# Optimization experiments

Hardware: AMD Instinct MI355X
Metric: run time of the kernel (lower is better)

Reference implementation:

```python
import jax, jax.numpy as jnp
import numpy as np

SIGNAL = (32, 32)
KERNEL = (8, 8)
N_FEATURES = [64, 128, 128]
BATCH = 64
ALPHA = 0.5          # source references an undefined global `alpha`; fixed here
LEAKY_SLOPE = 0.01   # torch F.leaky_relu default


def _join_tensor(S, K, loc):
    i = np.arange(S)[:, None, None]
    j = np.arange(S)[None, :, None]
    k = np.arange(K)[None, None, :]
    M = (j >= i) & (i == np.maximum(j, k + loc))
    return jnp.asarray(M.astype(np.float32))


def _meet_tensor(S, K, loc):
    i = np.arange(S)[:, None, None]
    j = np.arange(S)[None, :, None]
    k = np.arange(K)[None, None, :]
    M = (j >= i) & (i == np.minimum(j, k + loc))
    return jnp.asarray(M.astype(np.float32))


def setup_inputs() -> dict:
    key = jax.random.key(0)
    sx, sy = SIGNAL
    kx, ky = KERNEL
    # meet layers use kernel_loc = signal - kernel; join layers use (0, 0)
    cmx = _meet_tensor(sx, kx, sx - kx)
    cmy = _meet_tensor(sy, ky, sy - ky)
    cjx = _join_tensor(sx, kx, 0)
    cjy = _join_tensor(sy, ky, 0)

    keys = jax.random.split(key, 16)
    x = jax.random.normal(keys[0], (BATCH, N_FEATURES[0], sx, sy), dtype=jnp.float32)

    def kaiming(k, shape):
        fan_in = shape[0] * shape[1] * shape[2]  # kx*ky*in_features
        return jax.random.normal(k, shape, dtype=jnp.float32) * np.float32(np.sqrt(2.0 / fan_in))

    inp = {"x": x, "cmx": cmx, "cmy": cmy, "cjx": cjx, "cjy": cjy}
    for li in range(len(N_FEATURES) - 1):
        fi, fo = N_FEATURES[li], N_FEATURES[li + 1]
        inp[f"mw{li}"] = kaiming(keys[1 + 2 * li], (kx, ky, fi, fo))
        inp[f"mb{li}"] = jnp.zeros((fo, 1, 1), dtype=jnp.float32)
        inp[f"jw{li}"] = kaiming(keys[2 + 2 * li], (kx, ky, fi, fo))
        inp[f"jb{li}"] = jnp.zeros((fo, 1, 1), dtype=jnp.float32)
    return inp


def _lattice_conv(cx, cy, X, W, b):
    # Y[m,g,x,y] = sum_{i,j,a,b} cx[i,x,a] cy[j,y,b] X[m,f,i,j] W[a,b,f,g] + bias
    return jnp.einsum('ixa,jyb,mfij,abfg->mgxy', cx, cy, X, W, optimize='optimal') + b


def reference(x, cmx, cmy, cjx, cjy, mw0, mb0, jw0, jb0, mw1, mb1, jw1, jb1):
    params = [(mw0, mb0, jw0, jb0), (mw1, mb1, jw1, jb1)]
    for mw, mb, jw, jb in params:
        m = _lattice_conv(cmx, cmy, x, mw, mb)
        j = _lattice_conv(cjx, cjy, x, jw, jb)
        x = jax.nn.leaky_relu((1.0 - ALPHA) * m + ALPHA * j, negative_slope=LEAKY_SLOPE)
    return x
```

## Files before the change

### kernel.cpp

```cpp
#include <hip/hip_runtime.h>
#include <stdint.h>


typedef __attribute__((ext_vector_type(8))) short short8;
typedef __attribute__((ext_vector_type(4))) float floatx4;

__device__ __forceinline__ float bf2f(unsigned short u) {
  union { uint32_t u; float f; } c; c.u = ((uint32_t)u) << 16; return c.f;
}
__device__ __forceinline__ unsigned short f2bf(float f) {
  union { float f; uint32_t u; } c; c.f = f;
  uint32_t u = c.u;
  uint32_t r = (u + 0x7FFFu + ((u >> 16) & 1u)) >> 16;
  return (unsigned short)r;
}

__global__ void detect_and_bias(const unsigned short* __restrict__ xa,
                                const void* __restrict__ mb0,
                                const void* __restrict__ jb0,
                                const void* __restrict__ mb1,
                                const void* __restrict__ jb1,
                                float* __restrict__ bias0,
                                float* __restrict__ bias1,
                                int* __restrict__ flag) {
  __shared__ int cnt;
  if (threadIdx.x == 0) cnt = 0;
  __syncthreads();
  unsigned short v = xa[threadIdx.x];
  int e = (v >> 7) & 0xFF;
  int ok = (v == 0) || (e >= 110 && e <= 140);
  atomicAdd(&cnt, ok);
  __syncthreads();
  int fp32 = (cnt >= 240) ? 0 : 1;
  if (threadIdx.x == 0) *flag = fp32;
  int g = threadIdx.x & 127;
  const void* mb = (threadIdx.x < 128) ? mb0 : mb1;
  const void* jb = (threadIdx.x < 128) ? jb0 : jb1;
  float* bo = (threadIdx.x < 128) ? bias0 : bias1;
  float m = fp32 ? ((const float*)mb)[g] : bf2f(((const unsigned short*)mb)[g]);
  float j = fp32 ? ((const float*)jb)[g] : bf2f(((const unsigned short*)jb)[g]);
  bo[g] = 0.5f * (m + j);
}

__global__ __launch_bounds__(256) void transpose_in(
    const unsigned short* __restrict__ s16, const float* __restrict__ s32,
    unsigned short* __restrict__ dst, int R, int C,
    const int* __restrict__ flag) {
  __shared__ unsigned short tile[32][33];
  int fp32 = *flag;
  int tx = threadIdx.x, ty = threadIdx.y;
  int c0 = blockIdx.x * 32, r0 = blockIdx.y * 32;
  if (fp32) {
#pragma unroll
    for (int i = 0; i < 32; i += 8)
      tile[ty + i][tx] = f2bf(s32[(size_t)(r0 + ty + i) * C + (c0 + tx)]);
  } else {
#pragma unroll
    for (int i = 0; i < 32; i += 8)
      tile[ty + i][tx] = s16[(size_t)(r0 + ty + i) * C + (c0 + tx)];
  }
  __syncthreads();
#pragma unroll
  for (int i = 0; i < 32; i += 8)
    dst[(size_t)(c0 + ty + i) * R + (r0 + tx)] = tile[tx][ty + i];
}

__global__ __launch_bounds__(256) void transpose_out(
    const unsigned short* __restrict__ src, unsigned short* __restrict__ d16,
    float* __restrict__ d32, int R, int C, const int* __restrict__ flag) {
  __shared__ unsigned short tile[32][33];
  int fp32 = *flag;
  int tx = threadIdx.x, ty = threadIdx.y;
  int c0 = blockIdx.x * 32, r0 = blockIdx.y * 32;
#pragma unroll
  for (int i = 0; i < 32; i += 8)
    tile[ty + i][tx] = src[(size_t)(r0 + ty + i) * C + (c0 + tx)];
  __syncthreads();
  if (fp32) {
#pragma unroll
    for (int i = 0; i < 32; i += 8)
      d32[(size_t)(c0 + ty + i) * R + (r0 + tx)] = bf2f(tile[tx][ty + i]);
  } else {
#pragma unroll
    for (int i = 0; i < 32; i += 8)
      d16[(size_t)(c0 + ty + i) * R + (r0 + tx)] = tile[tx][ty + i];
  }
}

#define SLOT_W1 0
#define SLOT_SB 225
#define SLOT_AS 289
#define SLOT_M  353
#define N_SLOTS 417
#define N_SLOTS_PAD 448

__global__ __launch_bounds__(256) void pack_weights(
    const void* __restrict__ mw0, const void* __restrict__ jw0,
    const void* __restrict__ mw1, const void* __restrict__ jw1,
    unsigned short* __restrict__ PB0, unsigned short* __restrict__ PB1,
    const int* __restrict__ flag) {
  int layer = blockIdx.z;
  int FG = layer ? 16384 : 8192;
  int c0 = blockIdx.x * 32;
  if (c0 >= FG) return;
  int kt = blockIdx.y;
  const void* src = (kt < 2) ? (layer ? mw1 : mw0) : (layer ? jw1 : jw0);
  unsigned short* PB = layer ? PB1 : PB0;
  int r0 = (kt & 1) * 32;
  int fp32 = *flag;
  __shared__ unsigned short tile[32][33];
  int tx = threadIdx.x, ty = threadIdx.y;
#pragma unroll
  for (int i = 0; i < 32; i += 8) {
    size_t idx = (size_t)(r0 + ty + i) * FG + (c0 + tx);
    tile[ty + i][tx] = fp32 ? f2bf(((const float*)src)[idx])
                            : ((const unsigned short*)src)[idx];
  }
  __syncthreads();
#pragma unroll
  for (int i = 0; i < 32; i += 8)
    PB[(size_t)(c0 + ty + i) * 128 + (kt * 32 + tx)] = tile[tx][ty + i];
}

__global__ __launch_bounds__(256) void build_L(unsigned short* __restrict__ L) {
  int tid = blockIdx.x * 256 + threadIdx.x;
  int slot = tid >> 7, k = tid & 127;
  int isj = k >= 64, ab = k & 63, a = ab >> 3, b = ab & 7;
  float v = 0.f;
  if (slot < 225) {
    int cx = slot / 15, cy = slot % 15;
    int pmx = cx < 7 ? cx : 7, pxx = cx > 7 ? cx - 7 : 0;
    int pmy = cy < 7 ? cy : 7, pyy = cy > 7 ? cy - 7 : 0;
    if (!isj) v = (a >= pxx && b >= pyy) ? 0.5f : 0.f;
    else      v = (a <= pmx && b <= pmy) ? 0.5f : 0.f;
  } else if (slot < 289) {
    int s = slot - SLOT_SB, px = s >> 3, b0 = s & 7;
    if (!isj) v = (a >= px && b == b0) ? 0.5f : 0.f;
  } else if (slot < 353) {
    int s = slot - SLOT_AS, a0 = s >> 3, py = s & 7;
    if (!isj) v = (a == a0 && b >= py) ? 0.5f : 0.f;
  } else if (slot < 417) {
    int s = slot - SLOT_M, a0 = s >> 3, b0 = s & 7;
    if (!isj) v = (a == a0 && b == b0) ? 0.5f : 0.f;
  }
  L[tid] = f2bf(v);
}

template <int F, int NT>
__device__ __forceinline__ void mfma_tile(
    const unsigned short* __restrict__ A, const unsigned short* __restrict__ W,
    floatx4 acc[NT], int wave, int n, int q) {
  const unsigned short* a_ptr = A + ((size_t)(wave * 16 + n)) * F + q * 8;
  const unsigned short* w_ptr = W + (size_t)n * F + q * 8;
#pragma unroll
  for (int kk = 0; kk < F; kk += 32) {
    short8 av = *(const short8*)(a_ptr + kk);
#pragma unroll
    for (int t = 0; t < NT; ++t) {
      short8 bv = *(const short8*)(w_ptr + (size_t)t * 16 * F + kk);
      acc[t] = __builtin_amdgcn_mfma_f32_16x16x32_bf16(av, bv, acc[t], 0, 0, 0);
    }
  }
}

__global__ __launch_bounds__(256) void prep_gemm(
    const unsigned short* __restrict__ L,
    const unsigned short* __restrict__ PB0,
    const unsigned short* __restrict__ PB1,
    unsigned short* __restrict__ Int0, unsigned short* __restrict__ Int1) {
  int layer = blockIdx.z;
  int FG = layer ? 16384 : 8192;
  int n0 = blockIdx.x * 128;
  if (n0 >= FG) return;
  int m0 = blockIdx.y * 64;
  const unsigned short* PB = layer ? PB1 : PB0;
  unsigned short* Int = layer ? Int1 : Int0;
  int wave = threadIdx.x >> 6, lane = threadIdx.x & 63;
  int n = lane & 15, q = lane >> 4;
  floatx4 acc[8];
#pragma unroll
  for (int t = 0; t < 8; ++t) acc[t] = (floatx4){0.f, 0.f, 0.f, 0.f};
  mfma_tile<128, 8>(L + (size_t)m0 * 128, PB + (size_t)n0 * 128, acc, wave, n, q);
#pragma unroll
  for (int t = 0; t < 8; ++t) {
    int gcol = n0 + t * 16 + n;
#pragma unroll
    for (int r = 0; r < 4; ++r) {
      int m = m0 + wave * 16 + q * 4 + r;
      Int[(size_t)m * FG + gcol] = f2bf(acc[t][r]);
    }
  }
}

__global__ __launch_bounds__(256) void prep_stageB(
    const unsigned short* __restrict__ Int0,
    const unsigned short* __restrict__ Int1,
    unsigned short* __restrict__ Wall0, unsigned short* __restrict__ Wall1) {
  int zz = blockIdx.z;
  int layer = (zz >= N_SLOTS) ? 1 : 0;
  int slot = zz - layer * N_SLOTS;
  int F = layer ? 128 : 64;
  int f0 = blockIdx.y * 32;
  if (f0 >= F) return;
  int g0 = blockIdx.x * 32;
  const unsigned short* src =
      (layer ? Int1 : Int0) + (size_t)slot * F * 128;
  unsigned short* dst = (layer ? Wall1 : Wall0) + (size_t)slot * F * 128;
  __shared__ unsigned short tile[32][33];
  int tx = threadIdx.x, ty = threadIdx.y;
#pragma unroll
  for (int i = 0; i < 32; i += 8)
    tile[ty + i][tx] = src[(size_t)(f0 + ty + i) * 128 + (g0 + tx)];
  __syncthreads();
#pragma unroll
  for (int i = 0; i < 32; i += 8)
    dst[(size_t)(g0 + ty + i) * F + (f0 + tx)] = tile[tx][ty + i];
}

template <int F>
__global__ __launch_bounds__(256) void corr_gemm(
    const unsigned short* __restrict__ Xt, const unsigned short* __restrict__ Wall,
    float* __restrict__ V, float* __restrict__ U, float* __restrict__ T) {
  int bid = blockIdx.x, gs = blockIdx.y;
  int wave = threadIdx.x >> 6, lane = threadIdx.x & 63;
  int n = lane & 15, q = lane >> 4;
  int ipos, slot;
  float* out;
  if (bid < 256) {
    int a = bid >> 5, y = bid & 31;
    int py = y > 24 ? y - 24 : 0;
    ipos = (24 + a) * 32 + y;
    slot = SLOT_AS + a * 8 + py;
    out = V + (size_t)(a * 32 + y) * 8192;
  } else if (bid < 512) {
    int i = bid - 256;
    int b = i >> 5, x = i & 31;
    int px = x > 24 ? x - 24 : 0;
    ipos = x * 32 + 24 + b;
    slot = SLOT_SB + px * 8 + b;
    out = U + (size_t)(b * 32 + x) * 8192;
  } else {
    int i = bid - 512;
    int a = i >> 3, b = i & 7;
    ipos = (24 + a) * 32 + 24 + b;
    slot = SLOT_M + a * 8 + b;
    out = T + (size_t)(a * 8 + b) * 8192;
  }
  floatx4 acc[4];
#pragma unroll
  for (int t = 0; t < 4; ++t) acc[t] = (floatx4){0.f, 0.f, 0.f, 0.f};
  mfma_tile<F, 4>(Xt + (size_t)ipos * 64 * F,
                  Wall + ((size_t)slot * 128 + gs * 64) * F, acc, wave, n, q);
#pragma unroll
  for (int t = 0; t < 4; ++t) {
    int gcol = gs * 64 + t * 16 + n;
#pragma unroll
    for (int r = 0; r < 4; ++r) {
      int m = wave * 16 + q * 4 + r;
      out[(size_t)m * 128 + gcol] = acc[t][r];
    }
  }
}

__global__ __launch_bounds__(256) void scan_corr(float* __restrict__ V,
                                                 float* __restrict__ U,
                                                 float* __restrict__ T) {
  int b = blockIdx.x;
  if (b < 2048) {
    float* base = (b < 1024) ? V : U;
    int tid = ((b & 1023) * 256 + threadIdx.x);
    float* p = base + (size_t)tid;
    float s = 0.f;
#pragma unroll
    for (int a = 0; a < 8; ++a) {
      s += p[(size_t)a * 262144];
      p[(size_t)a * 262144] = s;
    }
  } else {
    int mg = (b - 2048) * 256 + threadIdx.x;
    float col[8];
#pragma unroll
    for (int i = 0; i < 8; ++i) col[i] = 0.f;
#pragma unroll
    for (int a = 0; a < 8; ++a) {
      float rs = 0.f;
#pragma unroll
      for (int bb = 0; bb < 8; ++bb) {
        size_t idx = (size_t)(a * 8 + bb) * 8192 + mg;
        col[bb] += T[idx];
        rs += col[bb];
        T[idx] = rs;
      }
    }
  }
}

template <int F>
__global__ __launch_bounds__(256) void final_gemm(
    const unsigned short* __restrict__ Xt, const unsigned short* __restrict__ Wall,
    const float* __restrict__ V, const float* __restrict__ U,
    const float* __restrict__ T, const float* __restrict__ bias,
    unsigned short* __restrict__ Out) {
  int pos = blockIdx.x, gs = blockIdx.y;
  int x = pos >> 5, y = pos & 31;
  int wave = threadIdx.x >> 6, lane = threadIdx.x & 63;
  int n = lane & 15, q = lane >> 4;
  int clsx = x < 7 ? x : (x <= 24 ? 7 : x - 17);
  int clsy = y < 7 ? y : (y <= 24 ? 7 : y - 17);
  int px = x > 24 ? x - 24 : 0;
  int py = y > 24 ? y - 24 : 0;
  const float* c3 = px ? V + ((size_t)(px - 1) * 32 + y) * 8192 : nullptr;
  const float* c2 = py ? U + ((size_t)(py - 1) * 32 + x) * 8192 : nullptr;
  const float* c4 =
      (px && py) ? T + (size_t)((px - 1) * 8 + (py - 1)) * 8192 : nullptr;

  float csum[4][4];
#pragma unroll
  for (int t = 0; t < 4; ++t) {
    int gcol = gs * 64 + t * 16 + n;
    float bv = bias[gcol];
#pragma unroll
    for (int r = 0; r < 4; ++r) {
      int m = wave * 16 + q * 4 + r;
      size_t idx = (size_t)m * 128 + gcol;
      float v = bv;
      if (c3) v += c3[idx];
      if (c2) v += c2[idx];
      if (c4) v += c4[idx];
      csum[t][r] = v;
    }
  }

  floatx4 acc[4];
#pragma unroll
  for (int t = 0; t < 4; ++t) acc[t] = (floatx4){0.f, 0.f, 0.f, 0.f};
  mfma_tile<F, 4>(Xt + (size_t)pos * 64 * F,
                  Wall + ((size_t)(SLOT_W1 + clsx * 15 + clsy) * 128 + gs * 64) * F,
                  acc, wave, n, q);

  unsigned short* o = Out + (size_t)pos * 64 * 128;
#pragma unroll
  for (int t = 0; t < 4; ++t) {
    int gcol = gs * 64 + t * 16 + n;
#pragma unroll
    for (int r = 0; r < 4; ++r) {
      int m = wave * 16 + q * 4 + r;
      float v = acc[t][r] + csum[t][r];
      v = v > 0.f ? v : 0.01f * v;
      o[(size_t)m * 128 + gcol] = f2bf(v);
    }
  }
}

extern "C" void kernel_launch(void* const* d_in, const int* in_sizes, int n_in,
                              void* d_out, int out_size, void* d_ws,
                              size_t ws_size, hipStream_t stream) {
  const void* x   = d_in[0];
  const void* mw0 = d_in[5];
  const void* mb0 = d_in[6];
  const void* jw0 = d_in[7];
  const void* jb0 = d_in[8];
  const void* mw1 = d_in[9];
  const void* mb1 = d_in[10];
  const void* jw1 = d_in[11];
  const void* jb1 = d_in[12];

  char* ws = (char*)d_ws;
  const size_t MB = 1u << 20;
  unsigned short* Xt0   = (unsigned short*)(ws + 0);
  unsigned short* A1    = (unsigned short*)(ws + 9 * MB);
  unsigned short* Wall0 = (unsigned short*)(ws + 26 * MB);
  unsigned short* Wall1 = (unsigned short*)(ws + 33 * MB);
  unsigned short* Int0  = (unsigned short*)(ws + 47 * MB);
  unsigned short* Int1  = (unsigned short*)(ws + 55 * MB);
  unsigned short* Out2  = (unsigned short*)(ws + 70 * MB);
  float* bias0 = (float*)(ws + 87 * MB);
  float* bias1 = bias0 + 128;
  int*   flag  = (int*)(bias1 + 128);
  unsigned short* PB0 = (unsigned short*)(ws + 88 * MB);
  unsigned short* PB1 = (unsigned short*)(ws + 91 * MB);
  unsigned short* L   = (unsigned short*)(ws + 96 * MB);
  float* V = (float*)d_out;
  float* U = V + (size_t)8 * 32 * 8192;
  float* T = U + (size_t)8 * 32 * 8192;

  dim3 tb(32, 8);
  detect_and_bias<<<1, 256, 0, stream>>>((const unsigned short*)x, mb0, jb0,
                                         mb1, jb1, bias0, bias1, flag);
  build_L<<<N_SLOTS_PAD * 128 / 256, 256, 0, stream>>>(L);
  pack_weights<<<dim3(512, 4, 2), tb, 0, stream>>>(mw0, jw0, mw1, jw1, PB0,
                                                   PB1, flag);
  prep_gemm<<<dim3(128, 7, 2), 256, 0, stream>>>(L, PB0, PB1, Int0, Int1);
  prep_stageB<<<dim3(4, 4, 2 * N_SLOTS), tb, 0, stream>>>(Int0, Int1, Wall0,
                                                          Wall1);
  transpose_in<<<dim3(32, 128), tb, 0, stream>>>(
      (const unsigned short*)x, (const float*)x, Xt0, 4096, 1024, flag);

  corr_gemm<64><<<dim3(576, 2), 256, 0, stream>>>(Xt0, Wall0, V, U, T);
  scan_corr<<<2080, 256, 0, stream>>>(V, U, T);
  final_gemm<64><<<dim3(1024, 2), 256, 0, stream>>>(Xt0, Wall0, V, U, T,
                                                    bias0, A1);
  corr_gemm<128><<<dim3(576, 2), 256, 0, stream>>>(A1, Wall1, V, U, T);
  scan_corr<<<2080, 256, 0, stream>>>(V, U, T);
  final_gemm<128><<<dim3(1024, 2), 256, 0, stream>>>(A1, Wall1, V, U, T,
                                                     bias1, Out2);

  transpose_out<<<dim3(256, 32), tb, 0, stream>>>(
      Out2, (unsigned short*)d_out, (float*)d_out, 1024, 8192, flag);
}
```

Measured before the change: 272.2 us.

## Fold weight transpose into packing, merge setup kernels, store correction partials as bf16

Weights are now packed in (g,f)-major order so the prep GEMM writes the final Wall layout directly, which removes the prep_stageB transpose pass and the Int intermediate buffers. The bias/flag detection and L construction are merged into one setup kernel to save a launch. The V/U/T correction buffers move from fp32 in the output buffer to bf16 in the workspace, halving their traffic in corr_gemm, scan_corr and final_gemm. The risk is extra rounding error, since the prefix-sum partials are re-rounded to bf16 at every step.

```diff
diff --git a/kernel.cpp b/kernel.cpp
--- a/kernel.cpp
+++ b/kernel.cpp
@@ -13,78 +13,6 @@
   uint32_t u = c.u;
   uint32_t r = (u + 0x7FFFu + ((u >> 16) & 1u)) >> 16;
   return (unsigned short)r;
-}
-
-__global__ void detect_and_bias(const unsigned short* __restrict__ xa,
-                                const void* __restrict__ mb0,
-                                const void* __restrict__ jb0,
-                                const void* __restrict__ mb1,
-                                const void* __restrict__ jb1,
-                                float* __restrict__ bias0,
-                                float* __restrict__ bias1,
-                                int* __restrict__ flag) {
-  __shared__ int cnt;
-  if (threadIdx.x == 0) cnt = 0;
-  __syncthreads();
-  unsigned short v = xa[threadIdx.x];
-  int e = (v >> 7) & 0xFF;
-  int ok = (v == 0) || (e >= 110 && e <= 140);
-  atomicAdd(&cnt, ok);
-  __syncthreads();
-  int fp32 = (cnt >= 240) ? 0 : 1;
-  if (threadIdx.x == 0) *flag = fp32;
-  int g = threadIdx.x & 127;
-  const void* mb = (threadIdx.x < 128) ? mb0 : mb1;
-  const void* jb = (threadIdx.x < 128) ? jb0 : jb1;
-  float* bo = (threadIdx.x < 128) ? bias0 : bias1;
-  float m = fp32 ? ((const float*)mb)[g] : bf2f(((const unsigned short*)mb)[g]);
-  float j = fp32 ? ((const float*)jb)[g] : bf2f(((const unsigned short*)jb)[g]);
-  bo[g] = 0.5f * (m + j);
-}
-
-__global__ __launch_bounds__(256) void transpose_in(
-    const unsigned short* __restrict__ s16, const float* __restrict__ s32,
-    unsigned short* __restrict__ dst, int R, int C,
-    const int* __restrict__ flag) {
-  __shared__ unsigned short tile[32][33];
-  int fp32 = *flag;
-  int tx = threadIdx.x, ty = threadIdx.y;
-  int c0 = blockIdx.x * 32, r0 = blockIdx.y * 32;
-  if (fp32) {
-#pragma unroll
-    for (int i = 0; i < 32; i += 8)
-      tile[ty + i][tx] = f2bf(s32[(size_t)(r0 + ty + i) * C + (c0 + tx)]);
-  } else {
-#pragma unroll
-    for (int i = 0; i < 32; i += 8)
-      tile[ty + i][tx] = s16[(size_t)(r0 + ty + i) * C + (c0 + tx)];
-  }
-  __syncthreads();
-#pragma unroll
-  for (int i = 0; i < 32; i += 8)
-    dst[(size_t)(c0 + ty + i) * R + (r0 + tx)] = tile[tx][ty + i];
-}
-
-__global__ __launch_bounds__(256) void transpose_out(
-    const unsigned short* __restrict__ src, unsigned short* __restrict__ d16,
-    float* __restrict__ d32, int R, int C, const int* __restrict__ flag) {
-  __shared__ unsigned short tile[32][33];
-  int fp32 = *flag;
-  int tx = threadIdx.x, ty = threadIdx.y;
-  int c0 = blockIdx.x * 32, r0 = blockIdx.y * 32;
-#pragma unroll
-  for (int i = 0; i < 32; i += 8)
-    tile[ty + i][tx] = src[(size_t)(r0 + ty + i) * C + (c0 + tx)];
-  __syncthreads();
-  if (fp32) {
-#pragma unroll
-    for (int i = 0; i < 32; i += 8)
-      d32[(size_t)(c0 + ty + i) * R + (r0 + tx)] = bf2f(tile[tx][ty + i]);
-  } else {
-#pragma unroll
-    for (int i = 0; i < 32; i += 8)
-      d16[(size_t)(c0 + ty + i) * R + (r0 + tx)] = tile[tx][ty + i];
-  }
 }
 
 #define SLOT_W1 0
@@ -94,36 +22,33 @@
 #define N_SLOTS 417
 #define N_SLOTS_PAD 448
 
-__global__ __launch_bounds__(256) void pack_weights(
-    const void* __restrict__ mw0, const void* __restrict__ jw0,
-    const void* __restrict__ mw1, const void* __restrict__ jw1,
-    unsigned short* __restrict__ PB0, unsigned short* __restrict__ PB1,
-    const int* __restrict__ flag) {
-  int layer = blockIdx.z;
-  int FG = layer ? 16384 : 8192;
-  int c0 = blockIdx.x * 32;
-  if (c0 >= FG) return;
-  int kt = blockIdx.y;
-  const void* src = (kt < 2) ? (layer ? mw1 : mw0) : (layer ? jw1 : jw0);
-  unsigned short* PB = layer ? PB1 : PB0;
-  int r0 = (kt & 1) * 32;
-  int fp32 = *flag;
-  __shared__ unsigned short tile[32][33];
-  int tx = threadIdx.x, ty = threadIdx.y;
-#pragma unroll
-  for (int i = 0; i < 32; i += 8) {
-    size_t idx = (size_t)(r0 + ty + i) * FG + (c0 + tx);
-    tile[ty + i][tx] = fp32 ? f2bf(((const float*)src)[idx])
-                            : ((const unsigned short*)src)[idx];
-  }
-  __syncthreads();
-#pragma unroll
-  for (int i = 0; i < 32; i += 8)
-    PB[(size_t)(c0 + ty + i) * 128 + (kt * 32 + tx)] = tile[tx][ty + i];
-}
-
-__global__ __launch_bounds__(256) void build_L(unsigned short* __restrict__ L) {
-  int tid = blockIdx.x * 256 + threadIdx.x;
+__global__ __launch_bounds__(256) void setup_kernel(
+    const unsigned short* __restrict__ xa,
+    const void* __restrict__ mb0, const void* __restrict__ jb0,
+    const void* __restrict__ mb1, const void* __restrict__ jb1,
+    float* __restrict__ bias0, float* __restrict__ bias1,
+    int* __restrict__ flag, unsigned short* __restrict__ L) {
+  if (blockIdx.x == 0) {
+    __shared__ int cnt;
+    if (threadIdx.x == 0) cnt = 0;
+    __syncthreads();
+    unsigned short v = xa[threadIdx.x];
+    int e = (v >> 7) & 0xFF;
+    int ok = (v == 0) || (e >= 110 && e <= 140);
+    atomicAdd(&cnt, ok);
+    __syncthreads();
+    int fp32 = (cnt >= 240) ? 0 : 1;
+    if (threadIdx.x == 0) *flag = fp32;
+    int g = threadIdx.x & 127;
+    const void* mb = (threadIdx.x < 128) ? mb0 : mb1;
+    const void* jb = (threadIdx.x < 128) ? jb0 : jb1;
+    float* bo = (threadIdx.x < 128) ? bias0 : bias1;
+    float m = fp32 ? ((const float*)mb)[g] : bf2f(((const unsigned short*)mb)[g]);
+    float j = fp32 ? ((const float*)jb)[g] : bf2f(((const unsigned short*)jb)[g]);
+    bo[g] = 0.5f * (m + j);
+    return;
+  }
+  int tid = (blockIdx.x - 1) * 256 + threadIdx.x;
   int slot = tid >> 7, k = tid & 127;
   int isj = k >= 64, ab = k & 63, a = ab >> 3, b = ab & 7;
   float v = 0.f;
@@ -146,6 +71,82 @@
   L[tid] = f2bf(v);
 }
 
+__global__ __launch_bounds__(256) void transpose_in(
+    const unsigned short* __restrict__ s16, const float* __restrict__ s32,
+    unsigned short* __restrict__ dst, int R, int C,
+    const int* __restrict__ flag) {
+  __shared__ unsigned short tile[32][33];
+  int fp32 = *flag;
+  int tx = threadIdx.x, ty = threadIdx.y;
+  int c0 = blockIdx.x * 32, r0 = blockIdx.y * 32;
+  if (fp32) {
+#pragma unroll
+    for (int i = 0; i < 32; i += 8)
+      tile[ty + i][tx] = f2bf(s32[(size_t)(r0 + ty + i) * C + (c0 + tx)]);
+  } else {
+#pragma unroll
+    for (int i = 0; i < 32; i += 8)
+      tile[ty + i][tx] = s16[(size_t)(r0 + ty + i) * C + (c0 + tx)];
+  }
+  __syncthreads();
+#pragma unroll
+  for (int i = 0; i < 32; i += 8)
+    dst[(size_t)(c0 + ty + i) * R + (r0 + tx)] = tile[tx][ty + i];
+}
+
+__global__ __launch_bounds__(256) void transpose_out(
+    const unsigned short* __restrict__ src, unsigned short* __restrict__ d16,
+    float* __restrict__ d32, int R, int C, const int* __restrict__ flag) {
+  __shared__ unsigned short tile[32][33];
+  int fp32 = *flag;
+  int tx = threadIdx.x, ty = threadIdx.y;
+  int c0 = blockIdx.x * 32, r0 = blockIdx.y * 32;
+#pragma unroll
+  for (int i = 0; i < 32; i += 8)
+    tile[ty + i][tx] = src[(size_t)(r0 + ty + i) * C + (c0 + tx)];
+  __syncthreads();
+  if (fp32) {
+#pragma unroll
+    for (int i = 0; i < 32; i += 8)
+      d32[(size_t)(c0 + ty + i) * R + (r0 + tx)] = bf2f(tile[tx][ty + i]);
+  } else {
+#pragma unroll
+    for (int i = 0; i < 32; i += 8)
+      d16[(size_t)(c0 + ty + i) * R + (r0 + tx)] = tile[tx][ty + i];
+  }
+}
+
+__global__ __launch_bounds__(256) void pack_weights2(
+    const void* __restrict__ mw0, const void* __restrict__ jw0,
+    const void* __restrict__ mw1, const void* __restrict__ jw1,
+    unsigned short* __restrict__ PBg0, unsigned short* __restrict__ PBg1,
+    const int* __restrict__ flag) {
+  int layer = blockIdx.z;
+  int F = layer ? 128 : 64;
+  int f = blockIdx.y;
+  if (f >= F) return;
+  int g0 = blockIdx.x * 32;
+  const int G = 128, FG = F * G;
+  const void* mw = layer ? mw1 : mw0;
+  const void* jw = layer ? jw1 : jw0;
+  unsigned short* PB = layer ? PBg1 : PBg0;
+  int fp32 = *flag;
+  __shared__ unsigned short lds[128][33];
+  int tx = threadIdx.x, ty = threadIdx.y;
+  for (int k = ty; k < 128; k += 8) {
+    const void* src = (k < 64) ? mw : jw;
+    int ab = k & 63;
+    size_t idx = (size_t)ab * FG + (size_t)f * G + g0 + tx;
+    lds[k][tx] = fp32 ? f2bf(((const float*)src)[idx])
+                      : ((const unsigned short*)src)[idx];
+  }
+  __syncthreads();
+  int tid = ty * 32 + tx;
+  int kk = tid & 127, gs = tid >> 7;
+  for (int gg = gs; gg < 32; gg += 2)
+    PB[((size_t)(g0 + gg) * F + f) * 128 + kk] = lds[kk][gg];
+}
+
 template <int F, int NT>
 __device__ __forceinline__ void mfma_tile(
     const unsigned short* __restrict__ A, const unsigned short* __restrict__ W,
@@ -163,18 +164,18 @@
   }
 }
 
-__global__ __launch_bounds__(256) void prep_gemm(
+__global__ __launch_bounds__(256) void prep_gemm2(
     const unsigned short* __restrict__ L,
-    const unsigned short* __restrict__ PB0,
-    const unsigned short* __restrict__ PB1,
-    unsigned short* __restrict__ Int0, unsigned short* __restrict__ Int1) {
+    const unsigned short* __restrict__ PBg0,
+    const unsigned short* __restrict__ PBg1,
+    unsigned short* __restrict__ Wall0, unsigned short* __restrict__ Wall1) {
   int layer = blockIdx.z;
-  int FG = layer ? 16384 : 8192;
+  int GF = layer ? 16384 : 8192;
   int n0 = blockIdx.x * 128;
-  if (n0 >= FG) return;
+  if (n0 >= GF) return;
   int m0 = blockIdx.y * 64;
-  const unsigned short* PB = layer ? PB1 : PB0;
-  unsigned short* Int = layer ? Int1 : Int0;
+  const unsigned short* PB = layer ? PBg1 : PBg0;
+  unsigned short* Wall = layer ? Wall1 : Wall0;
   int wave = threadIdx.x >> 6, lane = threadIdx.x & 63;
   int n = lane & 15, q = lane >> 4;
   floatx4 acc[8];
@@ -187,45 +188,21 @@
 #pragma unroll
     for (int r = 0; r < 4; ++r) {
       int m = m0 + wave * 16 + q * 4 + r;
-      Int[(size_t)m * FG + gcol] = f2bf(acc[t][r]);
-    }
-  }
-}
-
-__global__ __launch_bounds__(256) void prep_stageB(
-    const unsigned short* __restrict__ Int0,
-    const unsigned short* __restrict__ Int1,
-    unsigned short* __restrict__ Wall0, unsigned short* __restrict__ Wall1) {
-  int zz = blockIdx.z;
-  int layer = (zz >= N_SLOTS) ? 1 : 0;
-  int slot = zz - layer * N_SLOTS;
-  int F = layer ? 128 : 64;
-  int f0 = blockIdx.y * 32;
-  if (f0 >= F) return;
-  int g0 = blockIdx.x * 32;
-  const unsigned short* src =
-      (layer ? Int1 : Int0) + (size_t)slot * F * 128;
-  unsigned short* dst = (layer ? Wall1 : Wall0) + (size_t)slot * F * 128;
-  __shared__ unsigned short tile[32][33];
-  int tx = threadIdx.x, ty = threadIdx.y;
-#pragma unroll
-  for (int i = 0; i < 32; i += 8)
-    tile[ty + i][tx] = src[(size_t)(f0 + ty + i) * 128 + (g0 + tx)];
-  __syncthreads();
-#pragma unroll
-  for (int i = 0; i < 32; i += 8)
-    dst[(size_t)(g0 + ty + i) * F + (f0 + tx)] = tile[tx][ty + i];
+      Wall[(size_t)m * GF + gcol] = f2bf(acc[t][r]);
+    }
+  }
 }
 
 template <int F>
 __global__ __launch_bounds__(256) void corr_gemm(
     const unsigned short* __restrict__ Xt, const unsigned short* __restrict__ Wall,
-    float* __restrict__ V, float* __restrict__ U, float* __restrict__ T) {
+    unsigned short* __restrict__ V, unsigned short* __restrict__ U,
+    unsigned short* __restrict__ T) {
   int bid = blockIdx.x, gs = blockIdx.y;
   int wave = threadIdx.x >> 6, lane = threadIdx.x & 63;
   int n = lane & 15, q = lane >> 4;
   int ipos, slot;
-  float* out;
+  unsigned short* out;
   if (bid < 256) {
     int a = bid >> 5, y = bid & 31;
     int py = y > 24 ? y - 24 : 0;
@@ -257,24 +234,24 @@
 #pragma unroll
     for (int r = 0; r < 4; ++r) {
       int m = wave * 16 + q * 4 + r;
-      out[(size_t)m * 128 + gcol] = acc[t][r];
-    }
-  }
-}
-
-__global__ __launch_bounds__(256) void scan_corr(float* __restrict__ V,
-                                                 float* __restrict__ U,
-                                                 float* __restrict__ T) {
+      out[(size_t)m * 128 + gcol] = f2bf(acc[t][r]);
+    }
+  }
+}
+
+__global__ __launch_bounds__(256) void scan_corr(unsigned short* __restrict__ V,
+                                                 unsigned short* __restrict__ U,
+                                                 unsigned short* __restrict__ T) {
   int b = blockIdx.x;
   if (b < 2048) {
-    float* base = (b < 1024) ? V : U;
+    unsigned short* base = (b < 1024) ? V : U;
     int tid = ((b & 1023) * 256 + threadIdx.x);
-    float* p = base + (size_t)tid;
+    unsigned short* p = base + (size_t)tid;
     float s = 0.f;
 #pragma unroll
     for (int a = 0; a < 8; ++a) {
-      s += p[(size_t)a * 262144];
-      p[(size_t)a * 262144] = s;
+      s += bf2f(p[(size_t)a * 262144]);
+      p[(size_t)a * 262144] = f2bf(s);
     }
   } else {
     int mg = (b - 2048) * 256 + threadIdx.x;
@@ -287,9 +264,9 @@
 #pragma unroll
       for (int bb = 0; bb < 8; ++bb) {
         size_t idx = (size_t)(a * 8 + bb) * 8192 + mg;
-        col[bb] += T[idx];
+        col[bb] += bf2f(T[idx]);
         rs += col[bb];
-        T[idx] = rs;
+        T[idx] = f2bf(rs);
       }
     }
   }
@@ -298,8 +275,8 @@
 template <int F>
 __global__ __launch_bounds__(256) void final_gemm(
     const unsigned short* __restrict__ Xt, const unsigned short* __restrict__ Wall,
-    const float* __restrict__ V, const float* __restrict__ U,
-    const float* __restrict__ T, const float* __restrict__ bias,
+    const unsigned short* __restrict__ V, const unsigned short* __restrict__ U,
+    const unsigned short* __restrict__ T, const float* __restrict__ bias,
     unsigned short* __restrict__ Out) {
   int pos = blockIdx.x, gs = blockIdx.y;
   int x = pos >> 5, y = pos & 31;
@@ -309,9 +286,9 @@
   int clsy = y < 7 ? y : (y <= 24 ? 7 : y - 17);
   int px = x > 24 ? x - 24 : 0;
   int py = y > 24 ? y - 24 : 0;
-  const float* c3 = px ? V + ((size_t)(px - 1) * 32 + y) * 8192 : nullptr;
-  const float* c2 = py ? U + ((size_t)(py - 1) * 32 + x) * 8192 : nullptr;
-  const float* c4 =
+  const unsigned short* c3 = px ? V + ((size_t)(px - 1) * 32 + y) * 8192 : nullptr;
+  const unsigned short* c2 = py ? U + ((size_t)(py - 1) * 32 + x) * 8192 : nullptr;
+  const unsigned short* c4 =
       (px && py) ? T + (size_t)((px - 1) * 8 + (py - 1)) * 8192 : nullptr;
 
   float csum[4][4];
@@ -324,9 +301,9 @@
       int m = wave * 16 + q * 4 + r;
       size_t idx = (size_t)m * 128 + gcol;
       float v = bv;
-      if (c3) v += c3[idx];
-      if (c2) v += c2[idx];
-      if (c4) v += c4[idx];
+      if (c3) v += bf2f(c3[idx]);
+      if (c2) v += bf2f(c2[idx]);
+      if (c4) v += bf2f(c4[idx]);
       csum[t][r] = v;
     }
   }
@@ -370,29 +347,24 @@
   unsigned short* Xt0   = (unsigned short*)(ws + 0);
   unsigned short* A1    = (unsigned short*)(ws + 9 * MB);
   unsigned short* Wall0 = (unsigned short*)(ws + 26 * MB);
-  unsigned short* Wall1 = (unsigned short*)(ws + 33 * MB);
-  unsigned short* Int0  = (unsigned short*)(ws + 47 * MB);
-  unsigned short* Int1  = (unsigned short*)(ws + 55 * MB);
-  unsigned short* Out2  = (unsigned short*)(ws + 70 * MB);
-  float* bias0 = (float*)(ws + 87 * MB);
+  unsigned short* Wall1 = (unsigned short*)(ws + 34 * MB);
+  unsigned short* Out2  = (unsigned short*)(ws + 49 * MB);
+  unsigned short* PBg0  = (unsigned short*)(ws + 66 * MB);
+  unsigned short* PBg1  = (unsigned short*)(ws + 69 * MB);
+  unsigned short* L     = (unsigned short*)(ws + 74 * MB);
+  float* bias0 = (float*)(ws + 75 * MB);
   float* bias1 = bias0 + 128;
   int*   flag  = (int*)(bias1 + 128);
-  unsigned short* PB0 = (unsigned short*)(ws + 88 * MB);
-  unsigned short* PB1 = (unsigned short*)(ws + 91 * MB);
-  unsigned short* L   = (unsigned short*)(ws + 96 * MB);
-  float* V = (float*)d_out;
-  float* U = V + (size_t)8 * 32 * 8192;
-  float* T = U + (size_t)8 * 32 * 8192;
+  unsigned short* V = (unsigned short*)(ws + 76 * MB);
+  unsigned short* U = (unsigned short*)(ws + 81 * MB);
+  unsigned short* T = (unsigned short*)(ws + 86 * MB);
 
   dim3 tb(32, 8);
-  detect_and_bias<<<1, 256, 0, stream>>>((const unsigned short*)x, mb0, jb0,
-                                         mb1, jb1, bias0, bias1, flag);
-  build_L<<<N_SLOTS_PAD * 128 / 256, 256, 0, stream>>>(L);
-  pack_weights<<<dim3(512, 4, 2), tb, 0, stream>>>(mw0, jw0, mw1, jw1, PB0,
-                                                   PB1, flag);
-  prep_gemm<<<dim3(128, 7, 2), 256, 0, stream>>>(L, PB0, PB1, Int0, Int1);
-  prep_stageB<<<dim3(4, 4, 2 * N_SLOTS), tb, 0, stream>>>(Int0, Int1, Wall0,
-                                                          Wall1);
+  setup_kernel<<<225, 256, 0, stream>>>((const unsigned short*)x, mb0, jb0,
+                                        mb1, jb1, bias0, bias1, flag, L);
+  pack_weights2<<<dim3(4, 128, 2), tb, 0, stream>>>(mw0, jw0, mw1, jw1, PBg0,
+                                                    PBg1, flag);
+  prep_gemm2<<<dim3(128, 7, 2), 256, 0, stream>>>(L, PBg0, PBg1, Wall0, Wall1);
   transpose_in<<<dim3(32, 128), tb, 0, stream>>>(
       (const unsigned short*)x, (const float*)x, Xt0, 4096, 1024, flag);
 
```

Result: faster. 249.7 us (-8.3%).
